# Optimization experiments

Hardware: AMD Instinct MI355X
Metric: run time of the kernel (lower is better)

Reference implementation:

```python
import jax, jax.numpy as jnp
import numpy as np

B, S, D, F = 4, 2048, 1024, 4096

def setup_inputs() -> dict:
    key = jax.random.key(0)
    ks = jax.random.split(key, 6)
    return {
        "x": jax.random.normal(ks[0], (B, S, D), jnp.float32),
        "Qw": jax.random.normal(ks[1], (D, D), jnp.float32) / 40,
        "Kw": jax.random.normal(ks[2], (D, D), jnp.float32) / 40,
        "Vw": jax.random.normal(ks[3], (D, D), jnp.float32) / 40,
        "w1": jax.random.normal(ks[4], (D, F), jnp.float32) / 40,
        "b1": jnp.zeros((F,), jnp.float32),
        "w2": jax.random.normal(ks[5], (F, D), jnp.float32) / 40,
        "b2": jnp.zeros((D,), jnp.float32),
        "gamma1": jnp.ones((D,), jnp.float32),
        "beta1": jnp.zeros((D,), jnp.float32),
        "gamma2": jnp.ones((D,), jnp.float32),
        "beta2": jnp.zeros((D,), jnp.float32),
    }

def _layernorm(x, gamma, beta):
    num = x - jnp.mean(x, axis=-1, keepdims=True)
    den = jnp.sqrt(jnp.var(x, axis=-1, keepdims=True) + 1e-05)
    return gamma * (num / den) + beta

def _attention(x, Qw, Kw, Vw):
    Q, K, V = x @ Qw, x @ Kw, x @ Vw
    d = x.shape[-1]
    s = x.shape[-2]
    mask = jnp.where(jnp.tril(jnp.ones((s, s))) == 0, -jnp.inf, 0.0)
    scores = Q @ jnp.swapaxes(K, -1, -2) / jnp.sqrt(d) + mask
    return jax.nn.softmax(scores, axis=-1) @ V

def reference(x, Qw, Kw, Vw, w1, b1, w2, b2, gamma1, beta1, gamma2, beta2):
    x = x + _attention(_layernorm(x, gamma1, beta1), Qw, Kw, Vw)
    h = _layernorm(x, gamma2, beta2)
    x = x + (jax.nn.relu(h @ w1 + b1) @ w2 + b2)
    return x
```

## Files before the change

### kernel.cpp

```cpp
#include <hip/hip_runtime.h>
#include <hip/hip_bf16.h>

#define B_ 4
#define S_ 2048
#define D_ 1024
#define F_ 4096

typedef short bf16x8 __attribute__((ext_vector_type(8)));
typedef float f32x4 __attribute__((ext_vector_type(4)));

static __device__ __forceinline__ unsigned short f2bf(float f) {
    union { float f; unsigned int u; } v; v.f = f;
    unsigned int u = v.u + 0x7FFF + ((v.u >> 16) & 1);
    return (unsigned short)(u >> 16);
}
static __device__ __forceinline__ float bf2f(unsigned short u) {
    union { unsigned int u; float f; } v; v.u = ((unsigned int)u) << 16;
    return v.f;
}

typedef const __attribute__((address_space(1))) unsigned int* gp_t;
typedef __attribute__((address_space(3))) unsigned int* lp_t;
static __device__ __forceinline__ void gld16(const unsigned short* g, unsigned short* l) {
    __builtin_amdgcn_global_load_lds((gp_t)g, (lp_t)l, 16, 0, 0);
}

__global__ __launch_bounds__(256) void k_transpose_f32_bf16(
    const float* __restrict__ in, unsigned short* __restrict__ out, int R, int C) {
    __shared__ float t[32][33];
    int c0 = blockIdx.x * 32, r0 = blockIdx.y * 32;
    int x = threadIdx.x, y = threadIdx.y;
#pragma unroll
    for (int i = 0; i < 4; i++)
        t[y + 8 * i][x] = in[(size_t)(r0 + y + 8 * i) * C + c0 + x];
    __syncthreads();
#pragma unroll
    for (int i = 0; i < 4; i++)
        out[(size_t)(c0 + y + 8 * i) * R + r0 + x] = f2bf(t[x][y + 8 * i]);
}

__global__ __launch_bounds__(256) void k_transpose_w3(
    const float* __restrict__ Qw, const float* __restrict__ Kw, const float* __restrict__ Vw,
    unsigned short* __restrict__ out) {
    __shared__ float t[32][33];
    int z = blockIdx.z;
    const float* in = (z == 0) ? Qw : (z == 1) ? Kw : Vw;
    out += (size_t)z * D_ * D_;
    int c0 = blockIdx.x * 32, r0 = blockIdx.y * 32;
    int x = threadIdx.x, y = threadIdx.y;
#pragma unroll
    for (int i = 0; i < 4; i++)
        t[y + 8 * i][x] = in[(size_t)(r0 + y + 8 * i) * D_ + c0 + x];
    __syncthreads();
#pragma unroll
    for (int i = 0; i < 4; i++)
        out[(size_t)(c0 + y + 8 * i) * D_ + r0 + x] = f2bf(t[x][y + 8 * i]);
}

__global__ __launch_bounds__(256) void k_transpose_bf16(
    const unsigned short* __restrict__ in, unsigned short* __restrict__ out,
    int ldin, int ldout, long long szin, long long szout) {
    __shared__ unsigned short t[32][33];
    in += (long long)blockIdx.z * szin;
    out += (long long)blockIdx.z * szout;
    int c0 = blockIdx.x * 32, r0 = blockIdx.y * 32;
    int x = threadIdx.x, y = threadIdx.y;
#pragma unroll
    for (int i = 0; i < 4; i++)
        t[y + 8 * i][x] = in[(size_t)(r0 + y + 8 * i) * ldin + c0 + x];
    __syncthreads();
#pragma unroll
    for (int i = 0; i < 4; i++)
        out[(size_t)(c0 + y + 8 * i) * ldout + r0 + x] = t[x][y + 8 * i];
}

__global__ __launch_bounds__(256) void k_layernorm(
    const float* __restrict__ x, const float* __restrict__ gamma,
    const float* __restrict__ beta, unsigned short* __restrict__ out) {
    int row = blockIdx.x;
    int t = threadIdx.x;
    const float* xr = x + (size_t)row * D_;
    float4 v = ((const float4*)xr)[t];
    float s = v.x + v.y + v.z + v.w;
    float q = v.x * v.x + v.y * v.y + v.z * v.z + v.w * v.w;
#pragma unroll
    for (int off = 32; off; off >>= 1) {
        s += __shfl_down(s, off);
        q += __shfl_down(q, off);
    }
    __shared__ float ls[4], lq[4];
    int wv = t >> 6;
    if ((t & 63) == 0) { ls[wv] = s; lq[wv] = q; }
    __syncthreads();
    if (t == 0) {
        float S = ls[0] + ls[1] + ls[2] + ls[3];
        float Q = lq[0] + lq[1] + lq[2] + lq[3];
        float mean = S * (1.0f / D_);
        float var = Q * (1.0f / D_) - mean * mean;
        ls[0] = mean; lq[0] = rsqrtf(var + 1e-5f);
    }
    __syncthreads();
    float mean = ls[0], rstd = lq[0];
    float4 g = ((const float4*)gamma)[t];
    float4 b = ((const float4*)beta)[t];
    ushort4 o;
    o.x = f2bf(g.x * (v.x - mean) * rstd + b.x);
    o.y = f2bf(g.y * (v.y - mean) * rstd + b.y);
    o.z = f2bf(g.z * (v.z - mean) * rstd + b.z);
    o.w = f2bf(g.w * (v.w - mean) * rstd + b.w);
    ((ushort4*)(out + (size_t)row * D_))[t] = o;
}

__global__ __launch_bounds__(256) void k_softmax(unsigned short* __restrict__ sp) {
    int r = blockIdx.x;
    int i = r & (S_ - 1);
    unsigned short* row = sp + (size_t)r * S_;
    int t = threadIdx.x;
    int valid = i + 1;
    float vals[8];
    float mx = -1e30f;
#pragma unroll
    for (int k = 0; k < 8; k++) {
        int j = t + k * 256;
        vals[k] = (j < valid) ? bf2f(row[j]) : -1e30f;
        mx = fmaxf(mx, vals[k]);
    }
#pragma unroll
    for (int off = 32; off; off >>= 1) mx = fmaxf(mx, __shfl_xor(mx, off));
    __shared__ float red[4];
    if ((t & 63) == 0) red[t >> 6] = mx;
    __syncthreads();
    mx = fmaxf(fmaxf(red[0], red[1]), fmaxf(red[2], red[3]));
    __syncthreads();
    float e[8];
    float sum = 0.f;
#pragma unroll
    for (int k = 0; k < 8; k++) {
        int j = t + k * 256;
        e[k] = (j < valid) ? __expf(vals[k] - mx) : 0.f;
        sum += e[k];
    }
#pragma unroll
    for (int off = 32; off; off >>= 1) sum += __shfl_xor(sum, off);
    if ((t & 63) == 0) red[t >> 6] = sum;
    __syncthreads();
    sum = red[0] + red[1] + red[2] + red[3];
    float inv = 1.0f / sum;
#pragma unroll
    for (int k = 0; k < 8; k++) {
        int j = t + k * 256;
        row[j] = f2bf(e[k] * inv);
    }
}

template <int EPI>
__global__ __launch_bounds__(256) void k_gemm_bt(
    const unsigned short* __restrict__ A, const unsigned short* __restrict__ Bt,
    void* __restrict__ Cv, const float* __restrict__ bias, const float* __restrict__ res,
    int K, int lda, int ldb, int ldc,
    long long sA, long long sB, long long sC, float scale, int klimit, int swz) {
    int bn, bm, z;
    if (swz > 0) {
        int GN = gridDim.x, GM = gridDim.y;
        int L = blockIdx.x + GN * (blockIdx.y + GM * blockIdx.z);
        int rows = gridDim.y * gridDim.z;
        int xcd = L & 7;
        int s = L >> 3;
        int bng = GN / swz;
        int rpg = rows * swz / 8;
        int xg = xcd % swz, yg = xcd / swz;
        int bnl = s % bng;
        int rl = s / bng;
        int row = yg * rpg + rl;
        bn = xg * bng + bnl;
        bm = row % GM;
        z = row / GM;
    } else {
        bn = blockIdx.x; bm = blockIdx.y; z = blockIdx.z;
    }
    if (EPI == 1 && bn > bm) return;
    A += (long long)z * sA;
    Bt += (long long)z * sB;
    long long coff = (long long)z * sC;
    float* Cf = (float*)Cv;
    unsigned short* Cb = (unsigned short*)Cv;

    __shared__ unsigned short As[128 * 32];
    __shared__ unsigned short Bs[128 * 32];

    int t = threadIdx.x;
    int l = t & 63, w = t >> 6;
    int wm = (w & 1) * 64, wn = (w >> 1) * 64;
    int lr = l & 15, lq = l >> 4;

    f32x4 acc[4][4];
#pragma unroll
    for (int i = 0; i < 4; i++)
#pragma unroll
        for (int j = 0; j < 4; j++) acc[i][j] = (f32x4){0.f, 0.f, 0.f, 0.f};

    int kend = K;
    if (klimit) { int ke = (bm + 1) * 128; kend = ke < K ? ke : K; }

    int sr = l >> 2;
    int sc = (l & 3) * 8;
    const unsigned short* gA0 = A + (size_t)(bm * 128 + w * 32 + sr) * lda + sc;
    const unsigned short* gA1 = gA0 + (size_t)16 * lda;
    const unsigned short* gB0 = Bt + (size_t)(bn * 128 + w * 32 + sr) * ldb + sc;
    const unsigned short* gB1 = gB0 + (size_t)16 * ldb;
    unsigned short* lA0 = &As[(w * 32) * 32];
    unsigned short* lA1 = &As[(w * 32 + 16) * 32];
    unsigned short* lB0 = &Bs[(w * 32) * 32];
    unsigned short* lB1 = &Bs[(w * 32 + 16) * 32];

    for (int k0 = 0; k0 < kend; k0 += 32) {
        __syncthreads();
        gld16(gA0 + k0, lA0);
        gld16(gA1 + k0, lA1);
        gld16(gB0 + k0, lB0);
        gld16(gB1 + k0, lB1);
        __syncthreads();
        bf16x8 af[4], bf[4];
#pragma unroll
        for (int i = 0; i < 4; i++)
            af[i] = *(const bf16x8*)(&As[(wm + i * 16 + lr) * 32 + lq * 8]);
#pragma unroll
        for (int j = 0; j < 4; j++)
            bf[j] = *(const bf16x8*)(&Bs[(wn + j * 16 + lr) * 32 + lq * 8]);
#pragma unroll
        for (int i = 0; i < 4; i++)
#pragma unroll
            for (int j = 0; j < 4; j++)
                acc[i][j] = __builtin_amdgcn_mfma_f32_16x16x32_bf16(af[i], bf[j], acc[i][j], 0, 0, 0);
    }

#pragma unroll
    for (int i = 0; i < 4; i++) {
        int mbase = bm * 128 + wm + i * 16 + lq * 4;
#pragma unroll
        for (int j = 0; j < 4; j++) {
            int n = bn * 128 + wn + j * 16 + lr;
#pragma unroll
            for (int r = 0; r < 4; r++) {
                int m = mbase + r;
                float v = acc[i][j][r];
                long long idx = coff + (long long)m * ldc + n;
                if (EPI == 0) {
                    Cb[idx] = f2bf(v);
                } else if (EPI == 1) {
                    Cb[idx] = f2bf(v * scale);
                } else if (EPI == 2) {
                    Cf[idx] = v + res[idx];
                } else if (EPI == 3) {
                    float u = v + bias[n];
                    Cb[idx] = f2bf(u > 0.f ? u : 0.f);
                } else {
                    Cf[idx] = v + bias[n] + res[idx];
                }
            }
        }
    }
}

extern "C" void kernel_launch(void* const* d_in, const int* in_sizes, int n_in,
                              void* d_out, int out_size, void* d_ws, size_t ws_size,
                              hipStream_t stream) {
    const float* x      = (const float*)d_in[0];
    const float* Qw     = (const float*)d_in[1];
    const float* Kw     = (const float*)d_in[2];
    const float* Vw     = (const float*)d_in[3];
    const float* w1     = (const float*)d_in[4];
    const float* b1     = (const float*)d_in[5];
    const float* w2     = (const float*)d_in[6];
    const float* b2     = (const float*)d_in[7];
    const float* gamma1 = (const float*)d_in[8];
    const float* beta1  = (const float*)d_in[9];
    const float* gamma2 = (const float*)d_in[10];
    const float* beta2  = (const float*)d_in[11];
    float* out = (float*)d_out;

    char* ws = (char*)d_ws;
    size_t off = 0;
    auto alloc = [&](size_t bytes) -> void* {
        void* p = ws + off;
        off += (bytes + 255) & ~(size_t)255;
        return p;
    };
    const size_t MN = (size_t)B_ * S_ * D_;
    unsigned short* xn     = (unsigned short*)alloc(MN * 2);
    unsigned short* scoreP = (unsigned short*)alloc((size_t)B_ * S_ * S_ * 2);
    unsigned short* qkv    = (unsigned short*)alloc((size_t)B_ * S_ * 3072 * 2);
    unsigned short* VT     = (unsigned short*)alloc(MN * 2);
    unsigned short* QKVwT  = (unsigned short*)alloc((size_t)3 * D_ * D_ * 2);
    unsigned short* w1T    = (unsigned short*)alloc((size_t)D_ * F_ * 2);
    unsigned short* w2T    = (unsigned short*)alloc((size_t)F_ * D_ * 2);
    unsigned short* mid = qkv;

    dim3 tb(32, 8);
    k_transpose_w3<<<dim3(D_ / 32, D_ / 32, 3), tb, 0, stream>>>(Qw, Kw, Vw, QKVwT);
    k_transpose_f32_bf16<<<dim3(F_ / 32, D_ / 32), tb, 0, stream>>>(w1, w1T, D_, F_);
    k_transpose_f32_bf16<<<dim3(D_ / 32, F_ / 32), tb, 0, stream>>>(w2, w2T, F_, D_);

    k_layernorm<<<B_ * S_, 256, 0, stream>>>(x, gamma1, beta1, xn);

    const int Mtok = B_ * S_;
    k_gemm_bt<0><<<dim3(3072 / 128, Mtok / 128), 256, 0, stream>>>(
        xn, QKVwT, qkv, nullptr, nullptr, D_, D_, D_, 3072, 0, 0, 0, 1.f, 0, 4);

    k_transpose_bf16<<<dim3(D_ / 32, S_ / 32, B_), tb, 0, stream>>>(
        qkv + 2048, VT, 3072, S_, (long long)S_ * 3072, (long long)D_ * S_);

    k_gemm_bt<1><<<dim3(S_ / 128, S_ / 128, B_), 256, 0, stream>>>(
        qkv, qkv + 1024, scoreP, nullptr, nullptr, D_, 3072, 3072, S_,
        (long long)S_ * 3072, (long long)S_ * 3072, (long long)S_ * S_, 0.03125f, 0, 4);

    k_softmax<<<B_ * S_, 256, 0, stream>>>(scoreP);

    k_gemm_bt<2><<<dim3(D_ / 128, S_ / 128, B_), 256, 0, stream>>>(
        scoreP, VT, out, nullptr, x, S_, S_, S_, D_,
        (long long)S_ * S_, (long long)D_ * S_, (long long)S_ * D_, 1.f, 1, 2);

    k_layernorm<<<B_ * S_, 256, 0, stream>>>(out, gamma2, beta2, xn);

    k_gemm_bt<3><<<dim3(F_ / 128, Mtok / 128), 256, 0, stream>>>(
        xn, w1T, mid, b1, nullptr, D_, D_, D_, F_, 0, 0, 0, 1.f, 0, 4);

    k_gemm_bt<4><<<dim3(D_ / 128, Mtok / 128), 256, 0, stream>>>(
        mid, w2T, out, b2, out, F_, F_, F_, D_, 0, 0, 0, 1.f, 0, 2);
}
```

Baseline: 562.6 us.

## Double-buffer GEMM LDS tiles with 64-wide K stages and async waitcnt

```diff
diff --git a/kernel.cpp b/kernel.cpp
--- a/kernel.cpp
+++ b/kernel.cpp
@@ -24,6 +24,9 @@
 static __device__ __forceinline__ void gld16(const unsigned short* g, unsigned short* l) {
     __builtin_amdgcn_global_load_lds((gp_t)g, (lp_t)l, 16, 0, 0);
 }
+
+#define WAIT_VM8() __builtin_amdgcn_s_waitcnt(0x0F78)
+#define WAIT_VM0() __builtin_amdgcn_s_waitcnt(0x0F70)
 
 __global__ __launch_bounds__(256) void k_transpose_f32_bf16(
     const float* __restrict__ in, unsigned short* __restrict__ out, int R, int C) {
@@ -185,8 +188,8 @@
     float* Cf = (float*)Cv;
     unsigned short* Cb = (unsigned short*)Cv;
 
-    __shared__ unsigned short As[128 * 32];
-    __shared__ unsigned short Bs[128 * 32];
+    __shared__ unsigned short As[2][2][128 * 32];
+    __shared__ unsigned short Bs[2][2][128 * 32];
 
     int t = threadIdx.x;
     int l = t & 63, w = t >> 6;
@@ -208,30 +211,45 @@
     const unsigned short* gA1 = gA0 + (size_t)16 * lda;
     const unsigned short* gB0 = Bt + (size_t)(bn * 128 + w * 32 + sr) * ldb + sc;
     const unsigned short* gB1 = gB0 + (size_t)16 * ldb;
-    unsigned short* lA0 = &As[(w * 32) * 32];
-    unsigned short* lA1 = &As[(w * 32 + 16) * 32];
-    unsigned short* lB0 = &Bs[(w * 32) * 32];
-    unsigned short* lB1 = &Bs[(w * 32 + 16) * 32];
-
-    for (int k0 = 0; k0 < kend; k0 += 32) {
-        __syncthreads();
-        gld16(gA0 + k0, lA0);
-        gld16(gA1 + k0, lA1);
-        gld16(gB0 + k0, lB0);
-        gld16(gB1 + k0, lB1);
-        __syncthreads();
-        bf16x8 af[4], bf[4];
-#pragma unroll
-        for (int i = 0; i < 4; i++)
-            af[i] = *(const bf16x8*)(&As[(wm + i * 16 + lr) * 32 + lq * 8]);
-#pragma unroll
-        for (int j = 0; j < 4; j++)
-            bf[j] = *(const bf16x8*)(&Bs[(wn + j * 16 + lr) * 32 + lq * 8]);
-#pragma unroll
-        for (int i = 0; i < 4; i++)
+
+    auto stage = [&](int buf, int k0) {
+#pragma unroll
+        for (int kc = 0; kc < 2; kc++) {
+            int kk = k0 + kc * 32;
+            gld16(gA0 + kk, &As[buf][kc][(w * 32) * 32]);
+            gld16(gA1 + kk, &As[buf][kc][(w * 32 + 16) * 32]);
+            gld16(gB0 + kk, &Bs[buf][kc][(w * 32) * 32]);
+            gld16(gB1 + kk, &Bs[buf][kc][(w * 32 + 16) * 32]);
+        }
+    };
+
+    int NB = kend >> 6;
+    stage(0, 0);
+    for (int it = 0; it < NB; it++) {
+        int cur = it & 1;
+        if (it + 1 < NB) {
+            stage(1 - cur, (it + 1) * 64);
+            WAIT_VM8();
+        } else {
+            WAIT_VM0();
+        }
+        __builtin_amdgcn_s_barrier();
+#pragma unroll
+        for (int kc = 0; kc < 2; kc++) {
+            bf16x8 af[4], bf[4];
+#pragma unroll
+            for (int i = 0; i < 4; i++)
+                af[i] = *(const bf16x8*)(&As[cur][kc][(wm + i * 16 + lr) * 32 + lq * 8]);
 #pragma unroll
             for (int j = 0; j < 4; j++)
-                acc[i][j] = __builtin_amdgcn_mfma_f32_16x16x32_bf16(af[i], bf[j], acc[i][j], 0, 0, 0);
+                bf[j] = *(const bf16x8*)(&Bs[cur][kc][(wn + j * 16 + lr) * 32 + lq * 8]);
+#pragma unroll
+            for (int i = 0; i < 4; i++)
+#pragma unroll
+                for (int j = 0; j < 4; j++)
+                    acc[i][j] = __builtin_amdgcn_mfma_f32_16x16x32_bf16(af[i], bf[j], acc[i][j], 0, 0, 0);
+        }
+        __builtin_amdgcn_s_barrier();
     }
 
 #pragma unroll
```

Measured after the change: 480.8 us. 14.5% less time.
